# Kernel tuning notes

Hardware: AMD Instinct MI355X
Metric: run time of the kernel (lower is better)

Reference implementation:

```python
import jax, jax.numpy as jnp
import numpy as np
from jax import lax

B, T, C = 1, 2048, 2048
HS = 64
H = C // HS          # 32 heads
FFN = 7168
NS = 4               # packed sequences in the batch-1 stream
EPS_LN = 1e-5
EPS_GN = 1e-5 * 8 ** 2   # GroupNorm eps = 1e-5 * head_size_divisor**2


def setup_inputs() -> dict:
    key = jax.random.key(0)
    ks = iter(jax.random.split(key, 48))
    def rn(shape, s=1.0):
        return jax.random.normal(next(ks), shape, jnp.float32) * s
    sc = C ** -0.5
    return dict(
        x=rn((B, T, C)),
        start_pos=jnp.array([0, 512, 1024, 1536], dtype=jnp.int32),
        att_state=rn((NS, C)),
        wkv_state=rn((NS, H, HS, HS), 0.1),
        ffn_state=rn((NS, C)),
        ln1_g=jnp.ones((C,), jnp.float32), ln1_b=jnp.zeros((C,), jnp.float32),
        ln2_g=jnp.ones((C,), jnp.float32), ln2_b=jnp.zeros((C,), jnp.float32),
        tm_maa_x=rn((C,), 0.1), tm_maa_w=rn((C,), 0.1), tm_maa_k=rn((C,), 0.1),
        tm_maa_v=rn((C,), 0.1), tm_maa_r=rn((C,), 0.1), tm_maa_g=rn((C,), 0.1),
        tm_w1=rn((C, 160), 0.02), tm_w2=rn((5, 32, C), 0.02),
        td=rn((C,), 0.3) - 0.5, td_w1=rn((C, 64), 0.02), td_w2=rn((64, C), 0.02),
        u=rn((H, HS), 0.1),
        Wr=rn((C, C), sc), Wk=rn((C, C), sc), Wv=rn((C, C), sc),
        Wg=rn((C, C), sc), Wo=rn((C, C), sc),
        lnx_g=jnp.ones((C,), jnp.float32), lnx_b=jnp.zeros((C,), jnp.float32),
        cm_maa_k=rn((C,), 0.1), cm_maa_r=rn((C,), 0.1),
        Wck=rn((C, FFN), sc), Wcv=rn((FFN, C), FFN ** -0.5), Wcr=rn((C, C), sc),
    )


def _ln(x, g, b, eps):
    m = x.mean(-1, keepdims=True)
    v = ((x - m) ** 2).mean(-1, keepdims=True)
    return (x - m) * lax.rsqrt(v + eps) * g + b


def _shift(x, start_pos, state):
    # ZeroPad2d((0,0,1,-1)) token shift, then restore per-sequence carry state
    sh = jnp.concatenate([jnp.zeros_like(x[:, :1]), x[:, :-1]], axis=1)
    return sh.at[0, start_pos, :].set(state)


def reference(x, start_pos, att_state, wkv_state, ffn_state,
              ln1_g, ln1_b, ln2_g, ln2_b,
              tm_maa_x, tm_maa_w, tm_maa_k, tm_maa_v, tm_maa_r, tm_maa_g,
              tm_w1, tm_w2, td, td_w1, td_w2, u,
              Wr, Wk, Wv, Wg, Wo, lnx_g, lnx_b,
              cm_maa_k, cm_maa_r, Wck, Wcv, Wcr):
    is_start = jnp.zeros((T,), bool).at[start_pos].set(True)
    seq_id = jnp.clip(jnp.cumsum(is_start.astype(jnp.int32)) - 1, 0, NS - 1)

    # ---------------- Tmix (RWKV6 time mix) ----------------
    xa = _ln(x, ln1_g, ln1_b, EPS_LN)
    sh = _shift(xa, start_pos, att_state)
    xx = sh - xa
    xxx = jnp.tanh((xa + xx * tm_maa_x) @ tm_w1)                    # [B,T,160]
    mix = jnp.einsum('btse,sec->sbtc', xxx.reshape(B, T, 5, 32), tm_w2)
    mw, mk, mv, mr, mg = mix
    xw = xa + xx * (tm_maa_w + mw)
    xk = xa + xx * (tm_maa_k + mk)
    xv = xa + xx * (tm_maa_v + mv)
    xr = xa + xx * (tm_maa_r + mr)
    xg = xa + xx * (tm_maa_g + mg)
    r = (xr @ Wr).reshape(T, H, HS)
    k = (xk @ Wk).reshape(T, H, HS)
    v = (xv @ Wv).reshape(T, H, HS)
    g = jax.nn.silu(xg @ Wg)                                        # [B,T,C]
    w = td + jnp.tanh(xw @ td_w1) @ td_w2                           # [B,T,C]
    dec = jnp.exp(-jnp.exp(w)).reshape(T, H, HS)

    # continuous WKV recurrence: per-sequence state restore at starts
    def step(S, inp):
        rt, kt, vt, dt, st, sid = inp
        S = jnp.where(st, wkv_state[sid], S)                        # [H,HS,HS]
        y = jnp.einsum('hi,hij->hj', rt, S) \
            + (rt * u * kt).sum(-1, keepdims=True) * vt             # bonus term
        S = dt[:, :, None] * S + kt[:, :, None] * vt[:, None, :]
        return S, y

    _, y = lax.scan(step, jnp.zeros((H, HS, HS), jnp.float32),
                    (r, k, v, dec, is_start, seq_id))
    y = y.reshape(B, T, H, HS)
    # GroupNorm (n_head groups) fused per token/head
    mu = y.mean(-1, keepdims=True)
    var = ((y - mu) ** 2).mean(-1, keepdims=True)
    y = ((y - mu) * lax.rsqrt(var + EPS_GN)).reshape(B, T, C) * lnx_g + lnx_b
    x = x + (y * g) @ Wo

    # ---------------- CMix (channel mix) ----------------
    xf = _ln(x, ln2_g, ln2_b, EPS_LN)
    sh = _shift(xf, start_pos, ffn_state)
    xx = sh - xf
    xk = xf + xx * cm_maa_k
    xr = xf + xx * cm_maa_r
    kv = jnp.square(jax.nn.relu(xk @ Wck)) @ Wcv
    x = x + jax.nn.sigmoid(xr @ Wcr) * kv
    return x
```

## Files before the change

### kernel.cpp

```cpp
#include <hip/hip_runtime.h>
#include <stdint.h>


#define TT 2048
#define CC 2048
#define NH 32
#define HSZ 64
#define FFND 7168
#define CHUNK 32
#define NCHUNK 64

typedef __attribute__((ext_vector_type(8))) short short8;
typedef __attribute__((ext_vector_type(4))) float f32x4;

__device__ __forceinline__ float bf2f(short s){
  return __uint_as_float(((uint32_t)(uint16_t)s) << 16);
}
__device__ __forceinline__ short f2bf(float f){
  uint32_t u = __float_as_uint(f);
  u = u + 0x7fffu + ((u >> 16) & 1u);
  return (short)(u >> 16);
}

__global__ __launch_bounds__(256) void ln_kernel(
    const float* __restrict__ xin, const float* __restrict__ gam,
    const float* __restrict__ bet, float* __restrict__ out, float eps)
{
  int t = blockIdx.x, tid = threadIdx.x;
  const float* row = xin + (size_t)t*CC;
  float4 v0 = *(const float4*)(row + tid*8);
  float4 v1 = *(const float4*)(row + tid*8 + 4);
  float s  = v0.x+v0.y+v0.z+v0.w + v1.x+v1.y+v1.z+v1.w;
  float ss = v0.x*v0.x+v0.y*v0.y+v0.z*v0.z+v0.w*v0.w
           + v1.x*v1.x+v1.y*v1.y+v1.z*v1.z+v1.w*v1.w;
  #pragma unroll
  for(int off=1; off<64; off<<=1){ s += __shfl_xor(s,off); ss += __shfl_xor(ss,off); }
  __shared__ float sm[8];
  int w = tid>>6;
  if((tid&63)==0){ sm[w]=s; sm[4+w]=ss; }
  __syncthreads();
  s = sm[0]+sm[1]+sm[2]+sm[3]; ss = sm[4]+sm[5]+sm[6]+sm[7];
  float mean = s * (1.f/CC);
  float var  = ss * (1.f/CC) - mean*mean;
  float rstd = rsqrtf(var + eps);
  float* orow = out + (size_t)t*CC;
  int c = tid*8;
  float vv[8] = {v0.x,v0.y,v0.z,v0.w,v1.x,v1.y,v1.z,v1.w};
  #pragma unroll
  for(int j=0;j<8;j++) orow[c+j] = (vv[j]-mean)*rstd*gam[c+j] + bet[c+j];
}

__global__ __launch_bounds__(256) void ln2_fused_kernel(
    const float* __restrict__ p0, const float* __restrict__ p1,
    const float* __restrict__ xres, const float* __restrict__ gam,
    const float* __restrict__ bet, float* __restrict__ xsum,
    float* __restrict__ lnout, float eps)
{
  int t = blockIdx.x, tid = threadIdx.x;
  size_t base = (size_t)t*CC + tid*8;
  float vv[8];
  float s = 0.f, ss = 0.f;
  #pragma unroll
  for(int j=0;j<8;j++){
    float v = p0[base+j] + p1[base+j] + xres[base+j];
    vv[j] = v; s += v; ss += v*v;
    xsum[base+j] = v;
  }
  #pragma unroll
  for(int off=1; off<64; off<<=1){ s += __shfl_xor(s,off); ss += __shfl_xor(ss,off); }
  __shared__ float sm[8];
  int w = tid>>6;
  if((tid&63)==0){ sm[w]=s; sm[4+w]=ss; }
  __syncthreads();
  s = sm[0]+sm[1]+sm[2]+sm[3]; ss = sm[4]+sm[5]+sm[6]+sm[7];
  float mean = s * (1.f/CC);
  float var  = ss * (1.f/CC) - mean*mean;
  float rstd = rsqrtf(var + eps);
  int c = tid*8;
  #pragma unroll
  for(int j=0;j<8;j++) lnout[base+j] = (vv[j]-mean)*rstd*gam[c+j] + bet[c+j];
}

__global__ __launch_bounds__(256) void shift1_kernel(
    const float* __restrict__ xa, const float* __restrict__ st,
    const int* __restrict__ sp, float* __restrict__ xxb)
{
  int t = blockIdx.x, tid = threadIdx.x;
  int sp0=sp[0], sp1=sp[1], sp2=sp[2], sp3=sp[3];
  bool is_start = (sp0==t)|(sp1==t)|(sp2==t)|(sp3==t);
  int sid = (sp0<=t)+(sp1<=t)+(sp2<=t)+(sp3<=t) - 1;
  sid = sid<0?0:(sid>3?3:sid);
  int c = tid*8;
  const float* src = is_start ? (st + (size_t)sid*CC + c)
                   : (t>0 ? xa + (size_t)(t-1)*CC + c : nullptr);
  const float* cur = xa + (size_t)t*CC + c;
  float* o = xxb + (size_t)t*CC + c;
  #pragma unroll
  for(int jj=0;jj<8;jj++){
    float sh = src ? src[jj] : 0.f;
    o[jj] = sh - cur[jj];
  }
}

__global__ __launch_bounds__(256) void shift2_kernel(
    const float* __restrict__ xf, const float* __restrict__ st,
    const int* __restrict__ sp, const float* __restrict__ cmk,
    const float* __restrict__ cmr, short* __restrict__ xk2, short* __restrict__ xr2)
{
  int t = blockIdx.x, tid = threadIdx.x;
  int sp0=sp[0], sp1=sp[1], sp2=sp[2], sp3=sp[3];
  bool is_start = (sp0==t)|(sp1==t)|(sp2==t)|(sp3==t);
  int sid = (sp0<=t)+(sp1<=t)+(sp2<=t)+(sp3<=t) - 1;
  sid = sid<0?0:(sid>3?3:sid);
  int c = tid*8;
  const float* src = is_start ? (st + (size_t)sid*CC + c)
                   : (t>0 ? xf + (size_t)(t-1)*CC + c : nullptr);
  const float* cur = xf + (size_t)t*CC + c;
  size_t ix = (size_t)t*CC + c;
  #pragma unroll
  for(int jj=0;jj<8;jj++){
    float xfv = cur[jj];
    float sh = src ? src[jj] : 0.f;
    float d = sh - xfv;
    xk2[ix+jj] = f2bf(xfv + d*cmk[c+jj]);
    xr2[ix+jj] = f2bf(xfv + d*cmr[c+jj]);
  }
}

__global__ __launch_bounds__(256) void zprep_kernel(const float* __restrict__ xa,
   const float* __restrict__ xx, const float* __restrict__ maa, short* __restrict__ z)
{
  size_t i = ((size_t)blockIdx.x*256 + threadIdx.x)*8;
  int c = (int)(i & (CC-1));
  #pragma unroll
  for(int j=0;j<8;j++) z[i+j] = f2bf(xa[i+j] + xx[i+j]*maa[c+j]);
}

__global__ __launch_bounds__(256) void mix5_kernel(
    const float* __restrict__ xxxb, const float* __restrict__ w2,
    const float* __restrict__ xa, const float* __restrict__ xxv,
    const float* __restrict__ mw, const float* __restrict__ mk,
    const float* __restrict__ mv, const float* __restrict__ mr,
    const float* __restrict__ mg,
    short* __restrict__ ow, short* __restrict__ ok, short* __restrict__ ov,
    short* __restrict__ orr, short* __restrict__ og)
{
  int t0 = (blockIdx.x >> 3) * 8;
  int c  = ((blockIdx.x & 7) << 8) + threadIdx.x;
  float acc[5][8];
  #pragma unroll
  for(int s=0;s<5;s++)
    #pragma unroll
    for(int tt=0;tt<8;tt++) acc[s][tt]=0.f;
  #pragma unroll
  for(int s=0;s<5;s++){
    for(int e=0;e<32;e++){
      float wv = w2[(size_t)(s*32+e)*CC + c];
      #pragma unroll
      for(int tt=0;tt<8;tt++)
        acc[s][tt] += xxxb[(size_t)(t0+tt)*160 + s*32 + e] * wv;
    }
  }
  float vmw=mw[c], vmk=mk[c], vmv=mv[c], vmr=mr[c], vmg=mg[c];
  #pragma unroll
  for(int tt=0;tt<8;tt++){
    size_t ix = (size_t)(t0+tt)*CC + c;
    float av = xa[ix], xv = xxv[ix];
    ow[ix]  = f2bf(av + xv*(vmw + acc[0][tt]));
    ok[ix]  = f2bf(av + xv*(vmk + acc[1][tt]));
    ov[ix]  = f2bf(av + xv*(vmv + acc[2][tt]));
    orr[ix] = f2bf(av + xv*(vmr + acc[3][tt]));
    og[ix]  = f2bf(av + xv*(vmg + acc[4][tt]));
  }
}

__global__ __launch_bounds__(256) void dec_kernel(
    const float* __restrict__ h1b, const float* __restrict__ tw2,
    const float* __restrict__ td, float* __restrict__ out)
{
  int t0 = (blockIdx.x >> 3) * 8;
  int c  = ((blockIdx.x & 7) << 8) + threadIdx.x;
  float acc[8] = {0,0,0,0,0,0,0,0};
  for(int e=0;e<64;e++){
    float wv = tw2[(size_t)e*CC + c];
    #pragma unroll
    for(int tt=0;tt<8;tt++) acc[tt] += h1b[(size_t)(t0+tt)*64 + e]*wv;
  }
  float tdc = td[c];
  #pragma unroll
  for(int tt=0;tt<8;tt++)
    out[(size_t)(t0+tt)*CC + c] = expf(-expf(tdc + acc[tt]));
}

template<int N, int NK>
__global__ __launch_bounds__(256) void tanh_reduce_kernel(
    const float* __restrict__ part, float* __restrict__ out)
{
  int idx = blockIdx.x*256 + threadIdx.x;
  int col = idx & (N-1);
  int row = idx >> (N==256 ? 8 : 7);
  float s = 0.f;
  #pragma unroll
  for(int z=0;z<8;z++) s += part[(size_t)z*TT*N + idx];
  if(col < NK) out[(size_t)row*NK + col] = tanhf(s);
}

__global__ __launch_bounds__(256) void transpose_f2bf_kernel(
    const float* __restrict__ W, short* __restrict__ Wt, int K, int N)
{
  __shared__ float tile[64][65];
  int n0 = blockIdx.x*64, k0 = blockIdx.y*64;
  int tid = threadIdx.x;
  #pragma unroll
  for(int q=0;q<16;q++){
    int ix = q*256 + tid;
    int r = ix >> 6, cc2 = ix & 63;
    tile[r][cc2] = (n0 + cc2 < N) ? W[(size_t)(k0+r)*N + n0 + cc2] : 0.f;
  }
  __syncthreads();
  #pragma unroll
  for(int q=0;q<16;q++){
    int ix = q*256 + tid;
    int r = ix >> 6, cc2 = ix & 63;
    Wt[(size_t)(n0+r)*K + k0 + cc2] = f2bf(tile[cc2][r]);
  }
}

struct WPtr4 { const float* w[4]; };
__global__ __launch_bounds__(256) void transpose4_f2bf_kernel(
    WPtr4 ws4, short* __restrict__ Wt)
{
  __shared__ float tile[64][65];
  int z = blockIdx.z;
  const float* W = ws4.w[z];
  short* dst = Wt + (size_t)z*CC*CC;
  int n0 = blockIdx.x*64, k0 = blockIdx.y*64;
  int tid = threadIdx.x;
  #pragma unroll
  for(int q=0;q<16;q++){
    int ix = q*256 + tid;
    int r = ix >> 6, cc2 = ix & 63;
    tile[r][cc2] = W[(size_t)(k0+r)*CC + n0 + cc2];
  }
  __syncthreads();
  #pragma unroll
  for(int q=0;q<16;q++){
    int ix = q*256 + tid;
    int r = ix >> 6, cc2 = ix & 63;
    dst[(size_t)(n0+r)*CC + k0 + cc2] = f2bf(tile[cc2][r]);
  }
}

__device__ __forceinline__ void load_lds16(const void* g, void* l){
  __builtin_amdgcn_global_load_lds(
      (const __attribute__((address_space(1))) uint32_t*)g,
      (__attribute__((address_space(3))) uint32_t*)l, 16, 0, 0);
}

template<int EPI>
__global__ __launch_bounds__(256) void gemm_bt_kernel(
    const short* __restrict__ A, const short* __restrict__ Bt,
    void* __restrict__ Cout, int M, int N, int Kstride, int Klen,
    long zA, long zB, long zC)
{
  __shared__ __align__(16) short As[128*64];
  __shared__ __align__(16) short Bs[128*64];
  int z = blockIdx.z;
  const short* A0 = A + (size_t)z*zA;
  const short* B0 = Bt + (size_t)z*zB;
  int tid = threadIdx.x;
  int w = tid >> 6, lane = tid & 63;
  int l16 = lane & 15, lhi = lane >> 4;
  int wr = w >> 1, wc = w & 1;
  int gx = gridDim.x;
  int nwg = gx*gridDim.y;
  int lin = blockIdx.y*gx + blockIdx.x;
  int wg = (lin & 7)*(nwg >> 3) + (lin >> 3);
  int bn = wg % gx, bm = wg / gx;
  const short* Ab = A0 + (size_t)bm*128*Kstride;
  const short* Bb = B0 + (size_t)bn*128*Kstride;
  int srow = w*8 + (lane>>3);
  int scol = lane & 7;
  f32x4 acc[4][4] = {};
  for(int kt=0; kt<Klen; kt+=64){
    __syncthreads();
    #pragma unroll
    for(int q=0;q<4;q++){
      int row = q*32 + srow;
      int c8 = scol ^ (row & 7);
      int ldsoff = (q*256 + w*64)*8;
      load_lds16(Ab + (size_t)row*Kstride + kt + c8*8, As + ldsoff);
      load_lds16(Bb + (size_t)row*Kstride + kt + c8*8, Bs + ldsoff);
    }
    __syncthreads();
    #pragma unroll
    for(int kk=0;kk<2;kk++){
      short8 af[4], bf[4];
      #pragma unroll
      for(int m=0;m<4;m++){
        int row = wr*64 + m*16 + l16;
        int slot = (kk*4 + lhi) ^ (row & 7);
        af[m] = *(const short8*)(As + row*64 + slot*8);
      }
      #pragma unroll
      for(int n=0;n<4;n++){
        int row = wc*64 + n*16 + l16;
        int slot = (kk*4 + lhi) ^ (row & 7);
        bf[n] = *(const short8*)(Bs + row*64 + slot*8);
      }
      #pragma unroll
      for(int m=0;m<4;m++){
        #pragma unroll
        for(int n=0;n<4;n++)
          acc[m][n] = __builtin_amdgcn_mfma_f32_16x16x32_bf16(af[m], bf[n], acc[m][n], 0, 0, 0);
      }
    }
  }
  int m0 = bm*128 + wr*64;
  int n0 = bn*128 + wc*64;
  #pragma unroll
  for(int m=0;m<4;m++){
    #pragma unroll
    for(int n=0;n<4;n++){
      #pragma unroll
      for(int jj=0;jj<4;jj++){
        int row = m0 + m*16 + lhi*4 + jj;
        int col = n0 + n*16 + l16;
        size_t ix = (size_t)row*N + col;
        float val = acc[m][n][jj];
        if constexpr (EPI==0){ ((short*)Cout)[(size_t)z*zC + ix] = f2bf(val); }
        else if constexpr (EPI==3){ float rv = fmaxf(val, 0.f); ((short*)Cout)[ix] = f2bf(rv*rv); }
        else if constexpr (EPI==5){ ((float*)Cout)[(size_t)z*zC + ix] = val; }
        else {
          short* o = (short*)Cout + (size_t)z*zC;
          o[ix] = (z==3) ? f2bf(val/(1.f+expf(-val))) : f2bf(val);
        }
      }
    }
  }
}

template<int EPI>
__global__ __launch_bounds__(512, 1) void gemm256_kernel(
    const short* __restrict__ A, const short* __restrict__ Bt,
    void* __restrict__ Cout, int M, int N, int Kstride, int Klen,
    long zA, long zB, long zC)
{
  __shared__ __align__(16) short As[2][256*64];
  __shared__ __align__(16) short Bs[2][256*64];
  int z = blockIdx.z;
  const short* A0 = A + (size_t)z*zA;
  const short* B0 = Bt + (size_t)z*zB;
  int tid = threadIdx.x;
  int w = tid >> 6, lane = tid & 63;
  int l16 = lane & 15, lhi = lane >> 4;
  int wr = w >> 2, wc = w & 3;
  int gx = gridDim.x;
  int nwg = gx*gridDim.y;
  int lin = blockIdx.y*gx + blockIdx.x;
  int wg = (lin & 7)*(nwg >> 3) + (lin >> 3);
  int bn = wg % gx, bm = wg / gx;
  const short* Ab = A0 + (size_t)bm*256*Kstride;
  const short* Bb = B0 + (size_t)bn*256*Kstride;
  int srow_w = w*8 + (lane>>3);
  int scol = lane & 7;
  f32x4 acc[8][4] = {};

  auto STG = [&](const short* src, short* dst, int half, int kt){
    #pragma unroll
    for(int q=0;q<2;q++){
      int row = half*128 + q*64 + srow_w;
      int c8 = scol ^ (row & 7);
      load_lds16(src + (size_t)row*Kstride + kt + c8*8,
                 dst + (half*128 + q*64 + w*8)*64);
    }
  };
  auto DSA = [&](const short* Ac, int p, short8 afr[2][2]){
    #pragma unroll
    for(int mm=0;mm<2;mm++)
      #pragma unroll
      for(int kk=0;kk<2;kk++){
        int row = wr*128 + (p*2+mm)*16 + l16;
        int slot = (kk*4 + lhi) ^ (row & 7);
        afr[mm][kk] = *(const short8*)(Ac + row*64 + slot*8);
      }
  };
  auto DSB = [&](const short* Bc, short8 bfr[4][2]){
    #pragma unroll
    for(int n=0;n<4;n++)
      #pragma unroll
      for(int kk=0;kk<2;kk++){
        int row = wc*64 + n*16 + l16;
        int slot = (kk*4 + lhi) ^ (row & 7);
        bfr[n][kk] = *(const short8*)(Bc + row*64 + slot*8);
      }
  };
  auto MM = [&](int p, short8 afr[2][2], short8 bfr[4][2]){
    __builtin_amdgcn_s_setprio(1);
    #pragma unroll
    for(int mm=0;mm<2;mm++)
      #pragma unroll
      for(int n=0;n<4;n++)
        #pragma unroll
        for(int kk=0;kk<2;kk++)
          acc[p*2+mm][n] = __builtin_amdgcn_mfma_f32_16x16x32_bf16(
              afr[mm][kk], bfr[n][kk], acc[p*2+mm][n], 0, 0, 0);
    __builtin_amdgcn_s_setprio(0);
  };
  #define PH_SYNC() do{ __builtin_amdgcn_s_barrier(); \
      asm volatile("s_waitcnt lgkmcnt(0)" ::: "memory"); \
      __builtin_amdgcn_sched_barrier(0); }while(0)
  #define PH_END() do{ __builtin_amdgcn_s_barrier(); \
      __builtin_amdgcn_sched_barrier(0); }while(0)

  int NT = Klen >> 6;
  int niter = NT >> 1;
  STG(Ab, &As[0][0], 0, 0); STG(Ab, &As[0][0], 1, 0);
  STG(Bb, &Bs[0][0], 0, 0); STG(Bb, &Bs[0][0], 1, 0);
  STG(Bb, &Bs[1][0], 0, 64); STG(Bb, &Bs[1][0], 1, 64);
  asm volatile("s_waitcnt vmcnt(4)" ::: "memory");
  __builtin_amdgcn_s_barrier();
  __builtin_amdgcn_sched_barrier(0);

  for(int i=0;i<niter;++i){
    int kt_o  = (2*i+1) << 6;
    int kt_e2 = (2*i+2) << 6;
    int kt_o2 = (2*i+3) << 6;
    bool st = (i+1 < niter);
    short8 bfr[4][2], afr[2][2];
    DSB(&Bs[0][0], bfr);
    DSA(&As[0][0], 0, afr);
    STG(Ab, &As[1][0], 0, kt_o);
    PH_SYNC(); MM(0, afr, bfr); PH_END();
    DSA(&As[0][0], 1, afr);
    STG(Ab, &As[1][0], 1, kt_o);
    PH_SYNC(); MM(1, afr, bfr); PH_END();
    DSA(&As[0][0], 2, afr);
    if(st) STG(Bb, &Bs[0][0], 0, kt_e2);
    PH_SYNC(); MM(2, afr, bfr); PH_END();
    DSA(&As[0][0], 3, afr);
    if(st) STG(Bb, &Bs[0][0], 1, kt_e2);
    asm volatile("s_waitcnt vmcnt(4)" ::: "memory");
    PH_SYNC(); MM(3, afr, bfr); PH_END();
    DSB(&Bs[1][0], bfr);
    DSA(&As[1][0], 0, afr);
    if(st) STG(Ab, &As[0][0], 0, kt_e2);
    PH_SYNC(); MM(0, afr, bfr); PH_END();
    DSA(&As[1][0], 1, afr);
    if(st) STG(Ab, &As[0][0], 1, kt_e2);
    PH_SYNC(); MM(1, afr, bfr); PH_END();
    DSA(&As[1][0], 2, afr);
    if(st) STG(Bb, &Bs[1][0], 0, kt_o2);
    PH_SYNC(); MM(2, afr, bfr); PH_END();
    DSA(&As[1][0], 3, afr);
    if(st) STG(Bb, &Bs[1][0], 1, kt_o2);
    asm volatile("s_waitcnt vmcnt(4)" ::: "memory");
    PH_SYNC(); MM(3, afr, bfr); PH_END();
  }
  #undef PH_SYNC
  #undef PH_END

  int m0 = bm*256 + wr*128;
  int n0 = bn*256 + wc*64;
  #pragma unroll
  for(int m=0;m<8;m++){
    #pragma unroll
    for(int n=0;n<4;n++){
      #pragma unroll
      for(int jj=0;jj<4;jj++){
        int row = m0 + m*16 + lhi*4 + jj;
        int col = n0 + n*16 + l16;
        size_t ix = (size_t)row*N + col;
        float val = acc[m][n][jj];
        if constexpr (EPI==3){ float rv = fmaxf(val, 0.f); ((short*)Cout)[ix] = f2bf(rv*rv); }
        else if constexpr (EPI==5){ ((float*)Cout)[(size_t)z*zC + ix] = val; }
        else {
          short* o = (short*)Cout + (size_t)z*zC;
          o[ix] = (z==3) ? f2bf(val/(1.f+expf(-val))) : f2bf(val);
        }
      }
    }
  }
}

__global__ __launch_bounds__(256) void wkv_chunk_kernel(
    const short* __restrict__ rb, const short* __restrict__ kb,
    const short* __restrict__ vb, const float* __restrict__ db,
    const float* __restrict__ wkv_state, const float* __restrict__ u,
    const int* __restrict__ sp,
    float* __restrict__ yb, short* __restrict__ rtb,
    float* __restrict__ Bc, float* __restrict__ Pc)
{
  int blk = blockIdx.x;
  int ch = blk >> 5;
  int h  = blk & 31;
  int tid = threadIdx.x;
  int a = tid & 3, j = tid >> 2;
  int w = tid >> 6, lane = tid & 63;
  __shared__ float sr[2][64], sk[2][64], suk[2][64], sv[2][64], sd[2][64];
  __shared__ float sp_[64];
  float u_reg = (w==1) ? u[h*64 + lane] : 0.f;
  if(tid < 64) sp_[tid] = 1.f;
  float S[16];
  #pragma unroll
  for(int ii=0;ii<16;ii++) S[ii]=0.f;
  int sp0=sp[0], sp1=sp[1], sp2=sp[2], sp3=sp[3];
  int tbase = ch*CHUNK;
  {
    size_t gb = (size_t)tbase*CC + h*64;
    if(w==0)      sr[0][lane] = bf2f(rb[gb+lane]);
    else if(w==1){ float kv_=bf2f(kb[gb+lane]); sk[0][lane]=kv_; suk[0][lane]=u_reg*kv_; }
    else if(w==2) sv[0][lane] = bf2f(vb[gb+lane]);
    else          sd[0][lane] = db[gb+lane];
  }
  __syncthreads();
  for(int tl=0; tl<CHUNK; ++tl){
    int t = tbase + tl;
    int buf = tl & 1;
    if(tl+1 < CHUNK){
      size_t nb = (size_t)(t+1)*CC + h*64;
      int b2_ = buf^1;
      if(w==0)      sr[b2_][lane] = bf2f(rb[nb+lane]);
      else if(w==1){ float kv_=bf2f(kb[nb+lane]); sk[b2_][lane]=kv_; suk[b2_][lane]=u_reg*kv_; }
      else if(w==2) sv[b2_][lane] = bf2f(vb[nb+lane]);
      else          sd[b2_][lane] = db[nb+lane];
    }
    size_t base = (size_t)t*CC + h*64;
    bool is_start = (sp0==t)|(sp1==t)|(sp2==t)|(sp3==t);
    if(is_start){
      int sid = (sp0<=t)+(sp1<=t)+(sp2<=t)+(sp3<=t) - 1;
      sid = sid<0?0:(sid>3?3:sid);
      const float* wsrc = wkv_state + (((size_t)sid*NH + h)*HSZ + a*16)*HSZ + j;
      #pragma unroll
      for(int ii=0;ii<16;ii++) S[ii] = wsrc[(size_t)ii*HSZ];
      if(tid < 64) sp_[tid] = 0.f;
    }
    float vj = sv[buf][j];
    float yp = 0.f, bp = 0.f;
    #pragma unroll
    for(int ii=0;ii<16;ii++){
      int i = a*16 + ii;
      float ri = sr[buf][i];
      yp += ri * S[ii];
      bp += ri * suk[buf][i];
    }
    yp += __shfl_xor(yp, 1); yp += __shfl_xor(yp, 2);
    bp += __shfl_xor(bp, 1); bp += __shfl_xor(bp, 2);
    if(a == 0) yb[base + j] = yp + bp*vj;
    if(tid < 64){
      rtb[base + tid] = f2bf(sr[buf][tid] * sp_[tid]);
      sp_[tid] *= sd[buf][tid];
    }
    #pragma unroll
    for(int ii=0;ii<16;ii++){
      int i = a*16 + ii;
      S[ii] = sd[buf][i]*S[ii] + sk[buf][i]*vj;
    }
    __syncthreads();
  }
  size_t cb = ((size_t)ch*NH + h)*HSZ*HSZ;
  #pragma unroll
  for(int ii=0;ii<16;ii++) Bc[cb + (size_t)(a*16+ii)*HSZ + j] = S[ii];
  if(tid < 64) Pc[((size_t)ch*NH + h)*HSZ + tid] = sp_[tid];
}

__global__ __launch_bounds__(256) void wkv_combine_kernel(
    float* __restrict__ BS, const float* __restrict__ Pc)
{
  int idx = blockIdx.x*256 + threadIdx.x;
  int hi = idx >> 6;
  float s = 0.f;
  for(int cc=0; cc<NCHUNK; ++cc){
    size_t ix = (size_t)cc*(NH*HSZ*HSZ) + idx;
    float b = BS[ix];
    BS[ix] = s;
    s = Pc[cc*(NH*HSZ) + hi]*s + b;
  }
}

__global__ __launch_bounds__(256) void wkv_corr_kernel(
    const short* __restrict__ rtb, const float* __restrict__ Sin, float* __restrict__ yb)
{
  int blk = blockIdx.x;
  int ch = blk >> 5, h = blk & 31;
  __shared__ float Ssm[64][64];
  __shared__ float Rsm[32][65];
  int tid = threadIdx.x;
  const float* Sp = Sin + (size_t)(ch*NH + h)*HSZ*HSZ;
  #pragma unroll
  for(int q=0;q<16;q++) ((float*)Ssm)[q*256+tid] = Sp[q*256+tid];
  #pragma unroll
  for(int q=0;q<8;q++){
    int ix = q*256 + tid;
    int tl = ix>>6, i = ix&63;
    Rsm[tl][i] = bf2f(rtb[(size_t)(ch*CHUNK+tl)*CC + h*64 + i]);
  }
  __syncthreads();
  int tl = tid >> 3;
  int jq = tid & 7;
  float acc[8];
  #pragma unroll
  for(int jj=0;jj<8;jj++) acc[jj]=0.f;
  for(int i=0;i<64;i++){
    float rv = Rsm[tl][i];
    #pragma unroll
    for(int jj=0;jj<8;jj++) acc[jj] += rv * Ssm[i][jq*8+jj];
  }
  #pragma unroll
  for(int jj=0;jj<8;jj++)
    yb[(size_t)(ch*CHUNK+tl)*CC + h*64 + jq*8+jj] += acc[jj];
}

__global__ __launch_bounds__(256) void gn_mul_kernel(
    const float* __restrict__ yb, const short* __restrict__ gb,
    const float* __restrict__ gam, const float* __restrict__ bet,
    short* __restrict__ yg)
{
  int t = blockIdx.x, tid = threadIdx.x;
  int w = tid >> 6, lane = tid & 63;
  for(int q=0;q<8;q++){
    int h = q*4 + w;
    int cc = h*64 + lane;
    float val = yb[(size_t)t*CC + cc];
    float s = val, ss = val*val;
    #pragma unroll
    for(int off=1;off<64;off<<=1){ s += __shfl_xor(s,off); ss += __shfl_xor(ss,off); }
    float mu = s*(1.f/64.f);
    float var = ss*(1.f/64.f) - mu*mu;
    float rstd = rsqrtf(var + 6.4e-4f);
    float o = (val-mu)*rstd*gam[cc] + bet[cc];
    yg[(size_t)t*CC + cc] = f2bf(o * bf2f(gb[(size_t)t*CC + cc]));
  }
}

__global__ __launch_bounds__(256) void final_kernel(
    const float* __restrict__ s0, const float* __restrict__ s1,
    const float* __restrict__ kv0, const float* __restrict__ kv1,
    const float* __restrict__ kv2, const float* __restrict__ kv3,
    float* __restrict__ out)
{
  size_t i = ((size_t)blockIdx.x*256 + threadIdx.x)*8;
  #pragma unroll
  for(int j=0;j<8;j++){
    float sv = s0[i+j] + s1[i+j];
    float sig = 1.f/(1.f + expf(-sv));
    out[i+j] = out[i+j] + sig*(kv0[i+j] + kv1[i+j] + kv2[i+j] + kv3[i+j]);
  }
}

extern "C" void kernel_launch(void* const* d_in, const int* in_sizes, int n_in,
                              void* d_out, int out_size, void* d_ws, size_t ws_size,
                              hipStream_t stream)
{
  (void)in_sizes; (void)n_in; (void)out_size;
  const float* x         = (const float*)d_in[0];
  const int*   sp        = (const int*)d_in[1];
  const float* att_state = (const float*)d_in[2];
  const float* wkv_state = (const float*)d_in[3];
  const float* ffn_state = (const float*)d_in[4];
  const float* ln1_g=(const float*)d_in[5],  *ln1_b=(const float*)d_in[6];
  const float* ln2_g=(const float*)d_in[7],  *ln2_b=(const float*)d_in[8];
  const float* maa_x=(const float*)d_in[9],  *maa_w=(const float*)d_in[10], *maa_k=(const float*)d_in[11];
  const float* maa_v=(const float*)d_in[12], *maa_r=(const float*)d_in[13], *maa_g=(const float*)d_in[14];
  const float* tm_w1=(const float*)d_in[15], *tm_w2=(const float*)d_in[16];
  const float* td=(const float*)d_in[17],    *td_w1=(const float*)d_in[18], *td_w2=(const float*)d_in[19];
  const float* u = (const float*)d_in[20];
  const float* Wr=(const float*)d_in[21], *Wk=(const float*)d_in[22], *Wv=(const float*)d_in[23];
  const float* Wg=(const float*)d_in[24], *Wo=(const float*)d_in[25];
  const float* lnx_g=(const float*)d_in[26], *lnx_b=(const float*)d_in[27];
  const float* cm_k=(const float*)d_in[28],  *cm_r=(const float*)d_in[29];
  const float* Wck=(const float*)d_in[30], *Wcv=(const float*)d_in[31], *Wcr=(const float*)d_in[32];

  char* ws = (char*)d_ws;
  const size_t SLOT  = (size_t)TT*CC*4;
  const size_t BSLOT = (size_t)TT*CC*2;
  const size_t WT_SZ = (size_t)4*CC*CC*2;
  const size_t NEED  = 6*SLOT + 10*BSLOT + WT_SZ + (4u<<20);
  if(ws_size < NEED) return;

  float* xa   = (float*)(ws + 0*SLOT);
  float* xxb  = (float*)(ws + 1*SLOT);
  float* zw   = (float*)(ws + 2*SLOT);
  float* decb = (float*)(ws + 3*SLOT);
  float* yb   = (float*)(ws + 4*SLOT);
  float* S5   = (float*)(ws + 5*SLOT);
  float* BS   = xa;
  float* xxxPart = zw;
  float* h1Part  = yb;
  short* bA   = (short*)(ws + 6*SLOT);
  short* bO   = (short*)(ws + 6*SLOT + 4*BSLOT);
  short* b1 = bO + 0*(TT*CC);
  short* b2 = bO + 1*(TT*CC);
  short* b3 = bO + 2*(TT*CC);
  short* b4 = bO + 3*(TT*CC);
  short* b5 = bO + 4*(TT*CC);
  short* b6 = bO + 5*(TT*CC);
  short* WT = (short*)(ws + 6*SLOT + 10*BSLOT);
  char*  aux = (char*)WT + WT_SZ;
  float* xxxb = (float*)(aux);
  float* h1b  = (float*)(aux + (2u<<20));
  float* Pc   = (float*)(aux + (5u<<19));
  float* xmid = (float*)d_out;

  dim3 B256(256), B512(512);
  const int NTC8 = TT*CC/8/256;

  ln_kernel<<<TT, B256, 0, stream>>>(x, ln1_g, ln1_b, xa, 1e-5f);
  shift1_kernel<<<TT, B256, 0, stream>>>(xa, att_state, sp, xxb);
  zprep_kernel<<<NTC8, B256, 0, stream>>>(xa, xxb, maa_x, bA);
  transpose_f2bf_kernel<<<dim3(4, CC/64), B256, 0, stream>>>(tm_w1, WT, CC, 160);
  gemm_bt_kernel<5><<<dim3(2, TT/128, 8), B256, 0, stream>>>(bA, WT, xxxPart, TT, 256, CC, 256,
      256, 256, (long)TT*256);
  tanh_reduce_kernel<256,160><<<TT, B256, 0, stream>>>(xxxPart, xxxb);
  mix5_kernel<<<NTC8, B256, 0, stream>>>(xxxb, tm_w2, xa, xxb,
      maa_w, maa_k, maa_v, maa_r, maa_g,
      b5, bA + 1*(TT*CC), bA + 2*(TT*CC), bA, bA + 3*(TT*CC));
  transpose_f2bf_kernel<<<dim3(2, CC/64), B256, 0, stream>>>(td_w1, WT, CC, 64);
  gemm_bt_kernel<5><<<dim3(1, TT/128, 8), B256, 0, stream>>>(b5, WT, h1Part, TT, 128, CC, 256,
      256, 256, (long)TT*128);
  tanh_reduce_kernel<128,64><<<TT/2, B256, 0, stream>>>(h1Part, h1b);
  dec_kernel<<<NTC8, B256, 0, stream>>>(h1b, td_w2, td, decb);

  WPtr4 w4; w4.w[0]=Wr; w4.w[1]=Wk; w4.w[2]=Wv; w4.w[3]=Wg;
  transpose4_f2bf_kernel<<<dim3(CC/64, CC/64, 4), B256, 0, stream>>>(w4, WT);
  gemm256_kernel<6><<<dim3(CC/256, TT/256, 4), B512, 0, stream>>>(bA, WT, b1, TT, CC, CC, CC,
      (long)TT*CC, (long)CC*CC, (long)TT*CC);

  wkv_chunk_kernel<<<NCHUNK*NH, B256, 0, stream>>>(b1, b2, b3, decb, wkv_state, u, sp,
                                                   yb, b5, BS, Pc);
  wkv_combine_kernel<<<NH*HSZ*HSZ/256, B256, 0, stream>>>(BS, Pc);
  wkv_corr_kernel<<<NCHUNK*NH, B256, 0, stream>>>(b5, BS, yb);
  gn_mul_kernel<<<TT, B256, 0, stream>>>(yb, b4, lnx_g, lnx_b, b6);

  transpose_f2bf_kernel<<<dim3(CC/64, CC/64), B256, 0, stream>>>(Wo, WT, CC, CC);
  gemm_bt_kernel<5><<<dim3(CC/128, TT/128, 2), B256, 0, stream>>>(b6, WT, yb, TT, CC, CC, 1024,
      1024, 1024, (long)TT*CC);
  ln2_fused_kernel<<<TT, B256, 0, stream>>>(yb, S5, x, ln2_g, ln2_b, xmid, zw, 1e-5f);

  shift2_kernel<<<TT, B256, 0, stream>>>(zw, ffn_state, sp, cm_k, cm_r, bA, bA + 1*(TT*CC));
  transpose_f2bf_kernel<<<dim3(FFND/64, CC/64), B256, 0, stream>>>(Wck, WT, CC, FFND);
  gemm256_kernel<3><<<dim3(FFND/256, TT/256, 1), B512, 0, stream>>>(bA, WT, b1, TT, FFND, CC, CC,
      0, 0, 0);
  transpose_f2bf_kernel<<<dim3(CC/64, FFND/64), B256, 0, stream>>>(Wcv, WT, FFND, CC);
  gemm256_kernel<5><<<dim3(CC/256, TT/256, 4), B512, 0, stream>>>(b1, WT, zw, TT, CC, FFND, 1792,
      1792, 1792, (long)TT*CC);
  transpose_f2bf_kernel<<<dim3(CC/64, CC/64), B256, 0, stream>>>(Wcr, WT, CC, CC);
  gemm_bt_kernel<5><<<dim3(CC/128, TT/128, 2), B256, 0, stream>>>(bA + 1*(TT*CC), WT, xa, TT, CC, CC, 1024,
      1024, 1024, (long)TT*CC);
  final_kernel<<<NTC8, B256, 0, stream>>>(xa, xxb, zw, decb, yb, S5, xmid);
}
```

Baseline: 699.1 us.

## Double-buffer register fragments so LDS reads overlap MFMA in GEMM main loop

Restructures the 256x256 bf16 GEMM main loop to ping-pong A and B register fragments, issuing the LDS reads for the next phase before the MFMAs of the current phase. Partial lgkmcnt waits replace the full lgkmcnt(0) drains, and the first fragments are prefetched before the loop. The goal is to hide LDS read latency behind matrix math. In exchange it raises register pressure and adds barriers per phase, so correctness depends on the new wait counts and barrier placement around buffer reuse.

Measured after the change: 861.9 us. 23.3% more time.

```diff
diff --git a/kernel.cpp b/kernel.cpp
--- a/kernel.cpp
+++ b/kernel.cpp
@@ -365,6 +365,7 @@
   int srow_w = w*8 + (lane>>3);
   int scol = lane & 7;
   f32x4 acc[8][4] = {};
+  short8 bfr0[4][2], bfr1[4][2], afrA[2][2], afrB[2][2];
 
   auto STG = [&](const short* src, short* dst, int half, int kt){
     #pragma unroll
@@ -407,58 +408,81 @@
               afr[mm][kk], bfr[n][kk], acc[p*2+mm][n], 0, 0, 0);
     __builtin_amdgcn_s_setprio(0);
   };
-  #define PH_SYNC() do{ __builtin_amdgcn_s_barrier(); \
-      asm volatile("s_waitcnt lgkmcnt(0)" ::: "memory"); \
-      __builtin_amdgcn_sched_barrier(0); }while(0)
-  #define PH_END() do{ __builtin_amdgcn_s_barrier(); \
-      __builtin_amdgcn_sched_barrier(0); }while(0)
+  #define SB()   __builtin_amdgcn_sched_barrier(0)
+  #define BAR()  __builtin_amdgcn_s_barrier()
+  #define LGKM(n) asm volatile("s_waitcnt lgkmcnt(" #n ")" ::: "memory")
+  #define VMC(n)  asm volatile("s_waitcnt vmcnt(" #n ")" ::: "memory")
 
   int NT = Klen >> 6;
   int niter = NT >> 1;
   STG(Ab, &As[0][0], 0, 0); STG(Ab, &As[0][0], 1, 0);
   STG(Bb, &Bs[0][0], 0, 0); STG(Bb, &Bs[0][0], 1, 0);
   STG(Bb, &Bs[1][0], 0, 64); STG(Bb, &Bs[1][0], 1, 64);
-  asm volatile("s_waitcnt vmcnt(4)" ::: "memory");
-  __builtin_amdgcn_s_barrier();
-  __builtin_amdgcn_sched_barrier(0);
+  VMC(4); BAR(); SB();
+  DSB(&Bs[0][0], bfr0); DSA(&As[0][0], 0, afrA);
 
   for(int i=0;i<niter;++i){
     int kt_o  = (2*i+1) << 6;
     int kt_e2 = (2*i+2) << 6;
     int kt_o2 = (2*i+3) << 6;
     bool st = (i+1 < niter);
-    short8 bfr[4][2], afr[2][2];
-    DSB(&Bs[0][0], bfr);
-    DSA(&As[0][0], 0, afr);
     STG(Ab, &As[1][0], 0, kt_o);
-    PH_SYNC(); MM(0, afr, bfr); PH_END();
-    DSA(&As[0][0], 1, afr);
+    BAR(); SB();
+    DSA(&As[0][0], 1, afrB);
+    LGKM(4); SB();
+    MM(0, afrA, bfr0);
+    BAR(); SB();
     STG(Ab, &As[1][0], 1, kt_o);
-    PH_SYNC(); MM(1, afr, bfr); PH_END();
-    DSA(&As[0][0], 2, afr);
+    BAR(); SB();
+    DSA(&As[0][0], 2, afrA);
+    LGKM(4); SB();
+    MM(1, afrB, bfr0);
+    BAR(); SB();
     if(st) STG(Bb, &Bs[0][0], 0, kt_e2);
-    PH_SYNC(); MM(2, afr, bfr); PH_END();
-    DSA(&As[0][0], 3, afr);
-    if(st) STG(Bb, &Bs[0][0], 1, kt_e2);
-    asm volatile("s_waitcnt vmcnt(4)" ::: "memory");
-    PH_SYNC(); MM(3, afr, bfr); PH_END();
-    DSB(&Bs[1][0], bfr);
-    DSA(&As[1][0], 0, afr);
+    BAR(); SB();
+    DSA(&As[0][0], 3, afrB);
+    LGKM(4); SB();
+    MM(2, afrA, bfr0);
+    BAR(); SB();
+    if(st){ STG(Bb, &Bs[0][0], 1, kt_e2); VMC(4); } else { VMC(0); }
+    BAR(); SB();
+    DSB(&Bs[1][0], bfr1);
+    DSA(&As[1][0], 0, afrA);
+    LGKM(12); SB();
+    MM(3, afrB, bfr0);
+    BAR(); SB();
     if(st) STG(Ab, &As[0][0], 0, kt_e2);
-    PH_SYNC(); MM(0, afr, bfr); PH_END();
-    DSA(&As[1][0], 1, afr);
+    BAR(); SB();
+    DSA(&As[1][0], 1, afrB);
+    LGKM(4); SB();
+    MM(0, afrA, bfr1);
+    BAR(); SB();
     if(st) STG(Ab, &As[0][0], 1, kt_e2);
-    PH_SYNC(); MM(1, afr, bfr); PH_END();
-    DSA(&As[1][0], 2, afr);
+    BAR(); SB();
+    DSA(&As[1][0], 2, afrA);
+    LGKM(4); SB();
+    MM(1, afrB, bfr1);
+    BAR(); SB();
     if(st) STG(Bb, &Bs[1][0], 0, kt_o2);
-    PH_SYNC(); MM(2, afr, bfr); PH_END();
-    DSA(&As[1][0], 3, afr);
-    if(st) STG(Bb, &Bs[1][0], 1, kt_o2);
-    asm volatile("s_waitcnt vmcnt(4)" ::: "memory");
-    PH_SYNC(); MM(3, afr, bfr); PH_END();
-  }
-  #undef PH_SYNC
-  #undef PH_END
+    BAR(); SB();
+    DSA(&As[1][0], 3, afrB);
+    LGKM(4); SB();
+    MM(2, afrA, bfr1);
+    BAR(); SB();
+    if(st){ STG(Bb, &Bs[1][0], 1, kt_o2); VMC(4); } else { VMC(0); }
+    BAR(); SB();
+    if(st){
+      DSB(&Bs[0][0], bfr0);
+      DSA(&As[0][0], 0, afrA);
+      LGKM(12); SB();
+    } else { LGKM(0); SB(); }
+    MM(3, afrB, bfr1);
+    BAR(); SB();
+  }
+  #undef SB
+  #undef BAR
+  #undef LGKM
+  #undef VMC
 
   int m0 = bm*256 + wr*128;
   int n0 = bn*256 + wc*64;
```
